# Optimization experiments

Measured on AMD Instinct MI355X. Metric: run time of the kernel, lower is better.

## Reference

```python
import jax, jax.numpy as jnp
import numpy as np

NUM_HEADS = 8
H_DIM = 24
COORDS_DIM = 3
NUM_W_PER_DIST = 8
BLOCK_SIZE = 128
N_HASHES = 3
N = 32768
HASH_DIM = H_DIM + (COORDS_DIM - 1) + 2  # q/k augmented with RPE coordinate terms


def layernorm(x, g, b, eps=1e-5):
    mu = x.mean(-1, keepdims=True)
    var = ((x - mu) ** 2).mean(-1, keepdims=True)
    return (x - mu) * jax.lax.rsqrt(var + eps) * g + b


def setup_inputs() -> dict:
    key = jax.random.key(0)
    ks = jax.random.split(key, 16)
    d, H = H_DIM, NUM_HEADS
    s = lambda i, shape, scale: jax.random.normal(ks[i], shape, jnp.float32) * scale
    return {
        "x": s(0, (N, d), 1.0),
        "coords": jax.random.uniform(ks[1], (N, COORDS_DIM), jnp.float32),
        "norm1_g": jnp.ones((d,), jnp.float32),
        "norm1_b": jnp.zeros((d,), jnp.float32),
        "Wq": s(2, (d, H * d), d ** -0.5),
        "Wk": s(3, (d, H * d), d ** -0.5),
        "Wv": s(4, (d, H * d), d ** -0.5),
        "w_rpe_W": s(5, (H * d, (COORDS_DIM - 1) * NUM_W_PER_DIST), 0.3),
        "Wo": s(6, (H * d, d), (H * d) ** -0.5),
        "bo": jnp.zeros((d,), jnp.float32),
        "norm2_g": jnp.ones((d,), jnp.float32),
        "norm2_b": jnp.zeros((d,), jnp.float32),
        "ff_W1": s(7, (d, d), d ** -0.5),
        "ff_b1": jnp.zeros((d,), jnp.float32),
        "ff_W2": s(8, (d, d), d ** -0.5),
        "ff_b2": jnp.zeros((d,), jnp.float32),
        "alphas": s(9, (N_HASHES, H, HASH_DIM), 1.0),  # E2LSH projection vectors
    }


def hept_attention(q, k, v, coords, w_rpe_W, alphas):
    # q,k,v: [n, H*d]. HEPT: fold RPE exp(-w*||dp||^2) into augmented q/k, then
    # n_hashes rounds of LSH sort + block-local attention, combined by softmax
    # over each round's log-normalizer (Reformer-style).
    n = q.shape[0]
    H, d, B = NUM_HEADS, H_DIM, BLOCK_SIZE
    nb = n // B
    q = q.reshape(n, H, d).transpose(1, 0, 2) * (d ** -0.5)  # [H,n,d]
    k = k.reshape(n, H, d).transpose(1, 0, 2)
    v = v.reshape(n, H, d).transpose(1, 0, 2)
    # per-head non-negative distance weights from w_rpe (mixture collapsed)
    Wm = w_rpe_W.reshape(H, d, COORDS_DIM - 1, NUM_W_PER_DIST)
    w = jnp.mean(Wm, axis=(1, 3)) ** 2                        # [H, c-1]
    p = coords[:, 1:]                                          # [n, c-1]
    sqn = jnp.einsum("hc,nc,nc->hn", w, p, p)                # w*||p||^2
    qp = jnp.sqrt(2.0) * jnp.sqrt(w)[:, None, :] * p[None]     # [H,n,c-1]
    ones = jnp.ones((H, n, 1), q.dtype)
    # q_hat.k_hat = q.k + 2*w*p_i.p_j - w|p_i|^2 - w|p_j|^2 = q.k - w*||p_i-p_j||^2
    q_hat = jnp.concatenate([q, qp, -sqn[..., None], ones], -1)  # [H,n,HASH_DIM]
    k_hat = jnp.concatenate([k, qp, ones, -sqn[..., None]], -1)
    outs, zs = [], []
    for r in range(N_HASHES):
        a = alphas[r]                                          # [H, HASH_DIM]
        iq = jnp.argsort(jnp.einsum("hne,he->hn", q_hat, a), -1)
        ik = jnp.argsort(jnp.einsum("hne,he->hn", k_hat, a), -1)
        qs = jnp.take_along_axis(q_hat, iq[..., None], 1).reshape(H, nb, B, -1)
        ks = jnp.take_along_axis(k_hat, ik[..., None], 1).reshape(H, nb, B, -1)
        vs = jnp.take_along_axis(v, ik[..., None], 1).reshape(H, nb, B, d)
        logits = jnp.einsum("hbqe,hbke->hbqk", qs, ks)         # [H,nb,B,B]
        z = jax.nn.logsumexp(logits, -1).reshape(H, n)
        o = jnp.einsum("hbqk,hbkd->hbqd", jax.nn.softmax(logits, -1), vs).reshape(H, n, d)
        inv = jnp.argsort(iq, -1)                              # unsort to input order
        outs.append(jnp.take_along_axis(o, inv[..., None], 1))
        zs.append(jnp.take_along_axis(z, inv, 1))
    wts = jax.nn.softmax(jnp.stack(zs), axis=0)[..., None]     # [R,H,n,1]
    out = (jnp.stack(outs) * wts).sum(0)                       # [H,n,d]
    return out.transpose(1, 0, 2).reshape(n, H * d)


def reference(x, coords, norm1_g, norm1_b, Wq, Wk, Wv, w_rpe_W, Wo, bo,
              norm2_g, norm2_b, ff_W1, ff_b1, ff_W2, ff_b2, alphas):
    xn = layernorm(x, norm1_g, norm1_b)
    q, k, v = xn @ Wq, xn @ Wk, xn @ Wv
    aggr = hept_attention(q, k, v, coords, w_rpe_W, alphas) @ Wo + bo
    x = x + aggr  # dropout is identity in eval mode
    h = layernorm(x, norm2_g, norm2_b)
    ff = jax.nn.relu(h @ ff_W1 + ff_b1) @ ff_W2 + ff_b2
    return x + ff
```

## Files before the change

kernel.cpp:

```cpp
#include <hip/hip_runtime.h>
#include <math.h>

#define NPT 32768
#define NH 8
#define HD 24
#define EDIM 28
#define NHASH 3
#define NSEG 48
#define NRH 24

typedef unsigned long long u64;
typedef unsigned short ushort;
typedef __attribute__((__vector_size__(8 * sizeof(short)))) short bf16x8;
typedef __attribute__((__vector_size__(4 * sizeof(float)))) float floatx4;
typedef __attribute__((__vector_size__(4 * sizeof(unsigned int)))) unsigned int uint32x4;

__device__ __forceinline__ ushort f2bf(float f) {
    unsigned u = __float_as_uint(f);
    unsigned r = u + 0x7FFF + ((u >> 16) & 1);
    return (ushort)(r >> 16);
}
__device__ __forceinline__ float us2f(ushort u) {
    return __uint_as_float(((unsigned)u) << 16);
}

__global__ __launch_bounds__(256) void k0b(
    const float* __restrict__ wrpe, const float* __restrict__ Wq,
    const float* __restrict__ Wk, const float* __restrict__ alphas,
    double* __restrict__ w64, double* __restrict__ cqp64,
    double* __restrict__ Aq, double* __restrict__ Ak, double* __restrict__ ct) {
    __shared__ double sw[16], sc[16];
    int t = threadIdx.x;
    if (t < 16) {
        int h = t >> 1, c = t & 1;
        double s = 0.0;
        for (int i = 0; i < 24; i++)
            for (int j = 0; j < 8; j++)
                s += (double)wrpe[(h * 24 + i) * 16 + c * 8 + j];
        double m = s / 192.0;
        sw[t] = m * m;
        sc[t] = sqrt(2.0) * fabs(m);
        w64[t] = sw[t];
        cqp64[t] = sc[t];
    }
    __syncthreads();
    const double QSCALE = 1.0 / sqrt(24.0);
    for (int idx = t; idx < 24 * NRH; idx += 256) {
        int i = idx / NRH, rh = idx % NRH;
        int h = rh & 7;
        double aq = 0.0, ak = 0.0;
        for (int e = 0; e < 24; e++) {
            double al = (double)alphas[rh * 28 + e];
            aq += (double)Wq[i * 192 + h * 24 + e] * al;
            ak += (double)Wk[i * 192 + h * 24 + e] * al;
        }
        Aq[idx] = aq * QSCALE;
        Ak[idx] = ak;
    }
    if (t < NRH) {
        int h = t & 7;
        ct[t * 4 + 0] = (double)alphas[t * 28 + 24] * sc[h * 2 + 0];
        ct[t * 4 + 1] = (double)alphas[t * 28 + 25] * sc[h * 2 + 1];
        ct[t * 4 + 2] = (double)alphas[t * 28 + 26];
        ct[t * 4 + 3] = (double)alphas[t * 28 + 27];
    }
}

__global__ __launch_bounds__(512) void k2s(
    const float* __restrict__ x, const float* __restrict__ n1g,
    const float* __restrict__ n1b, const float* __restrict__ coords,
    const double* __restrict__ Aq, const double* __restrict__ Ak,
    const double* __restrict__ ct, const double* __restrict__ w64,
    u64* __restrict__ keys, float* __restrict__ xnf) {
    __shared__ double sA[2][24][NRH];
    __shared__ double sCt[NRH][4];
    __shared__ double sW64[16];
    __shared__ double sGB[48];
    __shared__ double sXn[8][24];
    int t = threadIdx.x;
    for (int i = t; i < 24 * NRH; i += 512) sA[0][i / NRH][i % NRH] = Aq[i];
    for (int i = t; i < 24 * NRH; i += 512) sA[1][i / NRH][i % NRH] = Ak[i];
    for (int i = t; i < NRH * 4; i += 512) sCt[i / 4][i % 4] = ct[i];
    if (t < 16) sW64[t] = w64[t];
    if (t < 24) { sGB[t] = (double)n1g[t]; sGB[24 + t] = (double)n1b[t]; }
    __syncthreads();
    int wv = t >> 6, l = t & 63;
    for (int g = 0; g < 8; g++) {
        int n = blockIdx.x * 64 + g * 8 + wv;
        double xv = (l < 24) ? (double)x[(u64)n * 24 + l] : 0.0;
        double s = xv;
        s += __shfl_xor(s, 1); s += __shfl_xor(s, 2); s += __shfl_xor(s, 4);
        s += __shfl_xor(s, 8); s += __shfl_xor(s, 16);
        double mu = s / 24.0;
        double d = (l < 24) ? (xv - mu) : 0.0;
        double v2 = d * d;
        v2 += __shfl_xor(v2, 1); v2 += __shfl_xor(v2, 2); v2 += __shfl_xor(v2, 4);
        v2 += __shfl_xor(v2, 8); v2 += __shfl_xor(v2, 16);
        double rstd = 1.0 / sqrt(v2 / 24.0 + 1e-5);
        if (l < 24) {
            double xn = d * rstd * sGB[l] + sGB[24 + l];
            sXn[wv][l] = xn;
            xnf[(u64)n * 24 + l] = (float)xn;
        }
        double p0 = (double)coords[(u64)n * 3 + 1];
        double p1 = (double)coords[(u64)n * 3 + 2];
        if (l < 2 * NRH) {
            int qk = l / NRH, rh = l % NRH;
            int h = rh & 7;
            double sqn = sW64[2 * h] * p0 * p0 + sW64[2 * h + 1] * p1 * p1;
            double acc = sCt[rh][0] * p0 + sCt[rh][1] * p1;
            acc += qk ? (sCt[rh][2] - sqn * sCt[rh][3]) : (sCt[rh][3] - sqn * sCt[rh][2]);
            for (int i = 0; i < 24; i++) acc += sXn[wv][i] * sA[qk][i][rh];
            u64 u = (u64)__double_as_longlong(acc);
            if (u >> 63) u = ~u; else u |= 0x8000000000000000ULL;
            u64 key = (u & ~(u64)32767) | (u64)n;
            keys[(u64)l * NPT + n] = key;
        }
    }
}

__device__ __forceinline__ u64 shflx64(u64 v, int d) {
    int lo = __shfl_xor((int)(unsigned)v, d);
    int hi = __shfl_xor((int)(unsigned)(v >> 32), d);
    return ((u64)(unsigned)hi << 32) | (unsigned)lo;
}
__device__ __forceinline__ void cswap(u64& a, u64& b, bool up) {
    if ((a > b) == up) { u64 tmp = a; a = b; b = tmp; }
}
__device__ __forceinline__ u64* sslot(u64* s, int i) {
    int a = i << 3;
    a ^= ((a >> 9) & 7) << 4;
    return (u64*)((char*)s + a);
}
__device__ __forceinline__ void reg_passes(u64 e[8], int ib, int K, int jmax) {
    for (int j = jmax; j >= 1; j >>= 1) {
#pragma unroll
        for (int k = 0; k < 8; k++)
            if ((k & j) == 0) cswap(e[k], e[k | j], ((ib + k) & K) == 0);
    }
}
__device__ __forceinline__ void shfl_passes(u64 e[8], int t, int segoff, int K, int jhi, int jlo) {
    for (int j = jhi; j >= jlo; j >>= 1) {
        int d = j >> 3;
        bool lower = (t & d) == 0;
        bool up = ((segoff + ((t & ~d) << 3)) & K) == 0;
        bool keepmin = (lower == up);
#pragma unroll
        for (int k = 0; k < 8; k++) {
            u64 o = shflx64(e[k], d);
            bool ownsm = e[k] < o;
            e[k] = (ownsm == keepmin) ? e[k] : o;
        }
    }
}

#define K2P_PTS 32
#define INVLN2F 1.4426950408889634f
__global__ __launch_bounds__(1024) void k2p_sort(
    u64* keys,
    const float* __restrict__ xnf,
    const float* __restrict__ Wq, const float* __restrict__ Wk,
    const float* __restrict__ Wv, const float* __restrict__ coords,
    const double* __restrict__ w64, const double* __restrict__ cqp64,
    ushort* __restrict__ qhatB, ushort* __restrict__ khatB, ushort* __restrict__ varrB) {
    __shared__ __align__(16) char smem[65536];
    int t = threadIdx.x;
    if (blockIdx.x < 192) {
        u64* s = (u64*)smem;
        u64 gbase = (u64)blockIdx.x * 8192;
        int segoff = (int)(gbase & 32767);
        int ib = segoff + t * 8;
        u64 e[8];
#pragma unroll
        for (int k = 0; k < 8; k++) e[k] = keys[gbase + t * 8 + k];
        reg_passes(e, ib, 2, 1);
        reg_passes(e, ib, 4, 2);
        reg_passes(e, ib, 8, 4);
        for (int K = 16; K <= 512; K <<= 1) {
            shfl_passes(e, t, segoff, K, K >> 1, 8);
            reg_passes(e, ib, K, 4);
        }
#pragma unroll
        for (int k = 0; k < 8; k++) *sslot(s, t * 8 + k) = e[k];
        __syncthreads();
        for (int K = 1024; K <= 8192; K <<= 1) {
            for (int j = K >> 1; j >= 512; j >>= 1) {
                for (int p = t; p < 4096; p += 1024) {
                    int i = ((p & ~(j - 1)) << 1) | (p & (j - 1));
                    int i2 = i | j;
                    bool up = (((segoff + i) & K) == 0);
                    u64 a = *sslot(s, i), b = *sslot(s, i2);
                    if ((a > b) == up) { *sslot(s, i) = b; *sslot(s, i2) = a; }
                }
                __syncthreads();
            }
#pragma unroll
            for (int k = 0; k < 8; k++) e[k] = *sslot(s, t * 8 + k);
            shfl_passes(e, t, segoff, K, 256, 8);
            reg_passes(e, ib, K, 4);
            if (K < 8192) {
#pragma unroll
                for (int k = 0; k < 8; k++) *sslot(s, t * 8 + k) = e[k];
                __syncthreads();
            } else {
#pragma unroll
                for (int k = 0; k < 8; k++) keys[gbase + t * 8 + k] = e[k];
            }
        }
    } else {
        ushort* sT = (ushort*)smem;
        int n0 = (blockIdx.x - 192) * K2P_PTS;
        if (t < 576) {
            int m = t / 192, jj = t % 192;
            const float* W = (m == 0) ? Wq : ((m == 1) ? Wk : Wv);
            float wc[24];
#pragma unroll
            for (int i = 0; i < 24; i++) wc[i] = W[i * 192 + jj];
            const float scale = (m == 0) ? (float)(1.4426950408889634 / sqrt(24.0)) : 1.0f;
            int h = jj / 24, e = jj % 24;
            ushort* sbase = sT + ((m * 8 + h) * K2P_PTS) * 32 + e;
            for (int p = 0; p < K2P_PTS; p++) {
                int n = n0 + p;
                const float* xr = xnf + (u64)n * 24;
                float acc = 0.f;
#pragma unroll
                for (int i = 0; i < 24; i++) acc += xr[i] * wc[i];
                sbase[p * 32] = f2bf(acc * scale);
            }
        } else if (t < 640) {
            int l = t - 576;
            int h2 = l >> 3, e2 = 24 + (l & 7);
            double c0 = cqp64[h2 * 2], c1 = cqp64[h2 * 2 + 1];
            double wa = w64[h2 * 2], wb = w64[h2 * 2 + 1];
            ushort* qb = sT + ((0 * 8 + h2) * K2P_PTS) * 32 + e2;
            ushort* kb = sT + ((1 * 8 + h2) * K2P_PTS) * 32 + e2;
            ushort* vb = sT + ((2 * 8 + h2) * K2P_PTS) * 32 + e2;
            for (int p = 0; p < K2P_PTS; p++) {
                int n = n0 + p;
                double p0 = (double)coords[(u64)n * 3 + 1];
                double p1 = (double)coords[(u64)n * 3 + 2];
                float qv, kv;
                if (e2 < 26) {
                    int c = e2 - 24;
                    float qp = (float)((c ? c1 : c0) * (c ? p1 : p0));
                    qv = qp; kv = qp;
                } else if (e2 < 28) {
                    double sqn = wa * p0 * p0 + wb * p1 * p1;
                    if (e2 == 26) { qv = (float)(-sqn); kv = 1.0f; }
                    else          { qv = 1.0f; kv = (float)(-sqn); }
                } else {
                    qv = 0.0f; kv = 0.0f;
                }
                qb[p * 32] = f2bf(qv * INVLN2F);
                kb[p * 32] = f2bf(kv);
                vb[p * 32] = 0;
            }
        }
        __syncthreads();
        for (int c = t; c < 3 * 8 * K2P_PTS * 4; c += 1024) {
            int arrh = c >> 7, off = c & 127;
            int arr = arrh >> 3, hh = arrh & 7;
            uint32x4 v = *(const uint32x4*)(sT + arrh * (K2P_PTS * 32) + off * 8);
            ushort* op = (arr == 0) ? qhatB : ((arr == 1) ? khatB : varrB);
            *(uint32x4*)(op + (u64)hh * NPT * 32 + (u64)n0 * 32 + off * 8) = v;
        }
    }
}

__global__ __launch_bounds__(1024) void sort_tail1_fused(u64* keys) {
    __shared__ u64 s[8192];
    int t = threadIdx.x;
    u64 gbase = (u64)blockIdx.x * 8192;
    u64 pbase = gbase ^ 8192ULL;
    int ci = (int)((gbase >> 13) & 3);
    bool keepmin = (ci == 0) || (ci == 3);
    int segoff = (int)(gbase & 32767);
    int ib = segoff + t * 8;
    for (int i = t; i < 8192; i += 1024) {
        u64 a = keys[gbase + i];
        u64 b = keys[pbase + i];
        u64 mn = a < b ? a : b;
        u64 mx = a < b ? b : a;
        *sslot(s, i) = keepmin ? mn : mx;
    }
    __syncthreads();
    const int K = 16384;
    for (int j = 4096; j >= 512; j >>= 1) {
        for (int p = t; p < 4096; p += 1024) {
            int i = ((p & ~(j - 1)) << 1) | (p & (j - 1));
            int i2 = i | j;
            bool up = (((segoff + i) & K) == 0);
            u64 a = *sslot(s, i), b = *sslot(s, i2);
            if ((a > b) == up) { *sslot(s, i) = b; *sslot(s, i2) = a; }
        }
        __syncthreads();
    }
    u64 e[8];
#pragma unroll
    for (int k = 0; k < 8; k++) e[k] = *sslot(s, t * 8 + k);
    shfl_passes(e, t, segoff, K, 256, 8);
    reg_passes(e, ib, K, 4);
#pragma unroll
    for (int k = 0; k < 8; k++) keys[gbase + t * 8 + k] = e[k];
}

__global__ __launch_bounds__(1024) void sort_local_tail(u64* keys, int K, int minj) {
    __shared__ u64 s[8192];
    int t = threadIdx.x;
    u64 gbase = (u64)blockIdx.x * 8192;
    int segoff = (int)(gbase & 32767);
    int ib = segoff + t * 8;
    for (int i = t; i < 8192; i += 1024) *sslot(s, i) = keys[gbase + i];
    __syncthreads();
    for (int j = 4096; j >= 512; j >>= 1) {
        for (int p = t; p < 4096; p += 1024) {
            int i = ((p & ~(j - 1)) << 1) | (p & (j - 1));
            int i2 = i | j;
            bool up = (((segoff + i) & K) == 0);
            u64 a = *sslot(s, i), b = *sslot(s, i2);
            if ((a > b) == up) { *sslot(s, i) = b; *sslot(s, i2) = a; }
        }
        __syncthreads();
    }
    u64 e[8];
#pragma unroll
    for (int k = 0; k < 8; k++) e[k] = *sslot(s, t * 8 + k);
    shfl_passes(e, t, segoff, K, 256, minj >= 8 ? minj : 8);
    if (minj < 8) reg_passes(e, ib, K, 4);
#pragma unroll
    for (int k = 0; k < 8; k++) keys[gbase + t * 8 + k] = e[k];
}

__global__ void sort_global2(u64* keys) {
    int p = blockIdx.x * blockDim.x + threadIdx.x;
    if (p >= NSEG * 8192) return;
    int seg = p >> 13, c = p & 8191;
    u64 base = (u64)seg * 32768 + c;
    u64 e0 = keys[base];
    u64 e1 = keys[base + 8192];
    u64 e2 = keys[base + 16384];
    u64 e3 = keys[base + 24576];
    u64 tmp;
    if (e0 > e2) { tmp = e0; e0 = e2; e2 = tmp; }
    if (e1 > e3) { tmp = e1; e1 = e3; e3 = tmp; }
    if (e0 > e1) { tmp = e0; e0 = e1; e1 = tmp; }
    if (e2 > e3) { tmp = e2; e2 = e3; e3 = tmp; }
    keys[base] = e0;
    keys[base + 8192] = e1;
    keys[base + 16384] = e2;
    keys[base + 24576] = e3;
}

__global__ __launch_bounds__(256, 4) void k3_attn(
    const u64* __restrict__ keys, const ushort* __restrict__ qhatB,
    const ushort* __restrict__ khatB, const ushort* __restrict__ varrB,
    ushort* __restrict__ ozB) {
    int rh3 = blockIdx.x % 24;
    int b = blockIdx.x / 24;
    int h = rh3 & 7, r = rh3 >> 3;
    __shared__ __align__(16) char smem[6144 + 32768 + 512];
    char* sVt = smem;
    char* sP  = smem + 6144;
    ushort* qidx = (ushort*)(smem + 6144 + 32768);
    ushort* kidx = qidx + 128;
    int t = threadIdx.x;
    int segQ = r * 8 + h, segK = 24 + r * 8 + h;
    if (t < 128) {
        qidx[t] = (ushort)(keys[(u64)segQ * NPT + b * 128 + t] & 32767ULL);
    } else {
        int i = t - 128;
        kidx[i] = (ushort)(keys[(u64)segK * NPT + b * 128 + i] & 32767ULL);
    }
    __syncthreads();

    int wave = t >> 6, L = t & 63;
    int quad = L >> 4, n16 = L & 15;

    const bf16x8* Qg = (const bf16x8*)(qhatB + (u64)h * NPT * 32);
    const bf16x8* Kg = (const bf16x8*)(khatB + (u64)h * NPT * 32);
    bf16x8 afr[2];
#pragma unroll
    for (int rtg = 0; rtg < 2; rtg++) {
        int qi = qidx[wave * 32 + rtg * 16 + n16];
        afr[rtg] = Qg[(u64)qi * 4 + quad];
    }
    bf16x8 bfr[8];
#pragma unroll
    for (int ct = 0; ct < 8; ct++) {
        int ki = kidx[ct * 16 + n16];
        bfr[ct] = Kg[(u64)ki * 4 + quad];
    }
    if (t < 128) {
        int ki = kidx[t];
        const bf16x8* vr = (const bf16x8*)(varrB + ((u64)h * NPT + ki) * 32);
        bf16x8 v0 = vr[0], v1 = vr[1], v2 = vr[2];
        int colb = ((t & 15) << 4) | ((t >> 4) << 1);
#pragma unroll
        for (int e = 0; e < 8; e++) {
            int e0 = e, e1 = 8 + e, e2 = 16 + e;
            *(short*)(sVt + e0 * 256 + (colb ^ ((e0 & 7) << 4))) = v0[e];
            *(short*)(sVt + e1 * 256 + (colb ^ ((e1 & 7) << 4))) = v1[e];
            *(short*)(sVt + e2 * 256 + (colb ^ ((e2 & 7) << 4))) = v2[e];
        }
    }
    __syncthreads();

    floatx4 acc[2][8];
#pragma unroll
    for (int rtg = 0; rtg < 2; rtg++)
#pragma unroll
        for (int ct = 0; ct < 8; ct++)
            acc[rtg][ct] = (floatx4){0.f, 0.f, 0.f, 0.f};
#pragma unroll
    for (int ct = 0; ct < 8; ct++) {
#pragma unroll
        for (int rtg = 0; rtg < 2; rtg++)
            acc[rtg][ct] = __builtin_amdgcn_mfma_f32_16x16x32_bf16(afr[rtg], bfr[ct], acc[rtg][ct], 0, 0, 0);
    }

    float mrow[2][4], srow[2][4];
#pragma unroll
    for (int rtg = 0; rtg < 2; rtg++) {
#pragma unroll
        for (int rg = 0; rg < 4; rg++) {
            float m = acc[rtg][0][rg];
#pragma unroll
            for (int ct = 1; ct < 8; ct++) m = fmaxf(m, acc[rtg][ct][rg]);
            m = fmaxf(m, __shfl_xor(m, 1));
            m = fmaxf(m, __shfl_xor(m, 2));
            m = fmaxf(m, __shfl_xor(m, 4));
            m = fmaxf(m, __shfl_xor(m, 8));
            mrow[rtg][rg] = m;
            float p[8];
            float s = 0.0f;
#pragma unroll
            for (int ct = 0; ct < 8; ct++) {
                p[ct] = exp2f(acc[rtg][ct][rg] - m);
                s += p[ct];
            }
            s += __shfl_xor(s, 1);
            s += __shfl_xor(s, 2);
            s += __shfl_xor(s, 4);
            s += __shfl_xor(s, 8);
            srow[rtg][rg] = s;
            unsigned w0, w1, w2, w3;
            asm("v_cvt_pk_bf16_f32 %0, %1, %2" : "=v"(w0) : "v"(p[0]), "v"(p[1]));
            asm("v_cvt_pk_bf16_f32 %0, %1, %2" : "=v"(w1) : "v"(p[2]), "v"(p[3]));
            asm("v_cvt_pk_bf16_f32 %0, %1, %2" : "=v"(w2) : "v"(p[4]), "v"(p[5]));
            asm("v_cvt_pk_bf16_f32 %0, %1, %2" : "=v"(w3) : "v"(p[6]), "v"(p[7]));
            int row = wave * 32 + rtg * 16 + quad * 4 + rg;
            uint32x4 pk = {w0, w1, w2, w3};
            *(uint32x4*)(sP + row * 256 + (((n16 << 4)) ^ ((row & 7) << 4))) = pk;
        }
    }

    floatx4 occ[2][2];
#pragma unroll
    for (int rtg = 0; rtg < 2; rtg++)
#pragma unroll
        for (int ct2 = 0; ct2 < 2; ct2++)
            occ[rtg][ct2] = (floatx4){0.f, 0.f, 0.f, 0.f};
#pragma unroll
    for (int ks = 0; ks < 4; ks++) {
        int kb = ks * 64 + quad * 16;
        bf16x8 bv[2], av[2];
#pragma unroll
        for (int ct2 = 0; ct2 < 2; ct2++) {
            int e = ct2 * 16 + n16;
            int ec = (e < 24) ? e : 0;
            bv[ct2] = *(const bf16x8*)(sVt + ec * 256 + (kb ^ ((ec & 7) << 4)));
        }
#pragma unroll
        for (int rtg = 0; rtg < 2; rtg++) {
            int rowA = wave * 32 + rtg * 16 + n16;
            av[rtg] = *(const bf16x8*)(sP + rowA * 256 + (kb ^ ((rowA & 7) << 4)));
        }
#pragma unroll
        for (int rtg = 0; rtg < 2; rtg++)
#pragma unroll
            for (int ct2 = 0; ct2 < 2; ct2++)
                occ[rtg][ct2] = __builtin_amdgcn_mfma_f32_16x16x32_bf16(av[rtg], bv[ct2], occ[rtg][ct2], 0, 0, 0);
    }

    const float LN2F = 0.6931471805599453f;
#pragma unroll
    for (int rtg = 0; rtg < 2; rtg++) {
#pragma unroll
        for (int rg = 0; rg < 4; rg++) {
            int row = wave * 32 + rtg * 16 + quad * 4 + rg;
            int oi = qidx[row];
            float inv = 1.0f / srow[rtg][rg];
            ushort* orow = ozB + ((u64)segQ * NPT + oi) * 32;
#pragma unroll
            for (int ct2 = 0; ct2 < 2; ct2++) {
                int col = ct2 * 16 + n16;
                if (col < 24) orow[col] = f2bf(occ[rtg][ct2][rg] * inv);
            }
            if (n16 == 0)
                *(float*)(orow + 24) = mrow[rtg][rg] * LN2F + __logf(srow[rtg][rg]);
        }
    }
}

#define K4PTS 32
#define AT_STR 196
#define W_STR 28
__global__ __launch_bounds__(256) void k4_final(
    const ushort* __restrict__ ozB,
    const float* __restrict__ x,
    const float* __restrict__ Wo, const float* __restrict__ bo,
    const float* __restrict__ g2, const float* __restrict__ b2,
    const float* __restrict__ W1, const float* __restrict__ b1f,
    const float* __restrict__ W2, const float* __restrict__ b2f,
    float* __restrict__ out) {
    __shared__ __align__(16) float sWoT[24][AT_STR];
    __shared__ __align__(16) float sW1T[24][W_STR], sW2T[24][W_STR];
    __shared__ float sB[5 * 24];
    __shared__ __align__(16) float attn[K4PTS][AT_STR];
    __shared__ float xrow[K4PTS][25];
    __shared__ __align__(16) float h2row[K4PTS][W_STR];
    __shared__ __align__(16) float ffrow[K4PTS][W_STR];
    int t = threadIdx.x;
    int base = blockIdx.x * K4PTS;
    for (int i = t; i < 4608; i += 256) sWoT[i % 24][i / 24] = Wo[i];
    for (int i = t; i < 576; i += 256) {
        sW1T[i % 24][i / 24] = W1[i];
        sW2T[i % 24][i / 24] = W2[i];
    }
    if (t < 24) {
        sB[t] = bo[t]; sB[24 + t] = g2[t]; sB[48 + t] = b2[t];
        sB[72 + t] = b1f[t]; sB[96 + t] = b2f[t];
    }
    if (t < K4PTS * 4) {
        int p = t >> 2, c = 24 + (t & 3);
        h2row[p][c] = 0.f; ffrow[p][c] = 0.f;
    }
    if (t < 24 * 4) {
        int rr = t >> 2, c = 24 + (t & 3);
        sW1T[rr][c] = 0.f; sW2T[rr][c] = 0.f;
    }
    {
        int p = t >> 3, h = t & 7;
        int n = base + p;
        const ushort* r0 = ozB + ((u64)(0 * 8 + h) * NPT + n) * 32;
        const ushort* r1 = ozB + ((u64)(1 * 8 + h) * NPT + n) * 32;
        const ushort* r2 = ozB + ((u64)(2 * 8 + h) * NPT + n) * 32;
        float z0 = *(const float*)(r0 + 24);
        float z1 = *(const float*)(r1 + 24);
        float z2 = *(const float*)(r2 + 24);
        float zm = fmaxf(z0, fmaxf(z1, z2));
        float e0 = __expf(z0 - zm), e1 = __expf(z1 - zm), e2 = __expf(z2 - zm);
        float inv = 1.0f / (e0 + e1 + e2);
        float w0 = e0 * inv, w1 = e1 * inv, w2 = e2 * inv;
#pragma unroll
        for (int e = 0; e < 24; e++)
            attn[p][h * 24 + e] = w0 * us2f(r0[e]) + w1 * us2f(r1[e]) + w2 * us2f(r2[e]);
    }
    __syncthreads();
    int p = t >> 3, oe = t & 7;
    int n = base + p;
    {
        const floatx4* ap = (const floatx4*)&attn[p][0];
        const floatx4* w0p = (const floatx4*)&sWoT[oe][0];
        const floatx4* w1p = (const floatx4*)&sWoT[oe + 8][0];
        const floatx4* w2p = (const floatx4*)&sWoT[oe + 16][0];
        floatx4 A0 = {0.f, 0.f, 0.f, 0.f}, A1 = A0, A2 = A0;
        for (int ii = 0; ii < 48; ii++) {
            floatx4 av = ap[ii];
            A0 += av * w0p[ii];
            A1 += av * w1p[ii];
            A2 += av * w2p[ii];
        }
        float a0 = A0[0] + A0[1] + A0[2] + A0[3];
        float a1 = A1[0] + A1[1] + A1[2] + A1[3];
        float a2 = A2[0] + A2[1] + A2[2] + A2[3];
        xrow[p][oe]      = x[n * 24 + oe]      + a0 + sB[oe];
        xrow[p][oe + 8]  = x[n * 24 + oe + 8]  + a1 + sB[oe + 8];
        xrow[p][oe + 16] = x[n * 24 + oe + 16] + a2 + sB[oe + 16];
    }
    float mu, rstd;
    {
        float s = xrow[p][oe] + xrow[p][oe + 8] + xrow[p][oe + 16];
        s += __shfl_xor(s, 1); s += __shfl_xor(s, 2); s += __shfl_xor(s, 4);
        mu = s / 24.0f;
        float v0 = xrow[p][oe] - mu, v1 = xrow[p][oe + 8] - mu, v2 = xrow[p][oe + 16] - mu;
        float v = v0 * v0 + v1 * v1 + v2 * v2;
        v += __shfl_xor(v, 1); v += __shfl_xor(v, 2); v += __shfl_xor(v, 4);
        rstd = 1.0f / sqrtf(v / 24.0f + 1e-5f);
    }
    h2row[p][oe]      = (xrow[p][oe] - mu)      * rstd * sB[24 + oe]      + sB[48 + oe];
    h2row[p][oe + 8]  = (xrow[p][oe + 8] - mu)  * rstd * sB[24 + oe + 8]  + sB[48 + oe + 8];
    h2row[p][oe + 16] = (xrow[p][oe + 16] - mu) * rstd * sB[24 + oe + 16] + sB[48 + oe + 16];
    {
        const floatx4* hp = (const floatx4*)&h2row[p][0];
        const floatx4* w0p = (const floatx4*)&sW1T[oe][0];
        const floatx4* w1p = (const floatx4*)&sW1T[oe + 8][0];
        const floatx4* w2p = (const floatx4*)&sW1T[oe + 16][0];
        floatx4 A0 = {0.f, 0.f, 0.f, 0.f}, A1 = A0, A2 = A0;
#pragma unroll
        for (int ii = 0; ii < 6; ii++) {
            floatx4 hv = hp[ii];
            A0 += hv * w0p[ii];
            A1 += hv * w1p[ii];
            A2 += hv * w2p[ii];
        }
        ffrow[p][oe]      = fmaxf(A0[0]+A0[1]+A0[2]+A0[3] + sB[72 + oe], 0.f);
        ffrow[p][oe + 8]  = fmaxf(A1[0]+A1[1]+A1[2]+A1[3] + sB[72 + oe + 8], 0.f);
        ffrow[p][oe + 16] = fmaxf(A2[0]+A2[1]+A2[2]+A2[3] + sB[72 + oe + 16], 0.f);
    }
    {
        const floatx4* fp = (const floatx4*)&ffrow[p][0];
        const floatx4* w0p = (const floatx4*)&sW2T[oe][0];
        const floatx4* w1p = (const floatx4*)&sW2T[oe + 8][0];
        const floatx4* w2p = (const floatx4*)&sW2T[oe + 16][0];
        floatx4 A0 = {0.f, 0.f, 0.f, 0.f}, A1 = A0, A2 = A0;
#pragma unroll
        for (int ii = 0; ii < 6; ii++) {
            floatx4 fv = fp[ii];
            A0 += fv * w0p[ii];
            A1 += fv * w1p[ii];
            A2 += fv * w2p[ii];
        }
        out[n * 24 + oe]      = xrow[p][oe]      + A0[0]+A0[1]+A0[2]+A0[3] + sB[96 + oe];
        out[n * 24 + oe + 8]  = xrow[p][oe + 8]  + A1[0]+A1[1]+A1[2]+A1[3] + sB[96 + oe + 8];
        out[n * 24 + oe + 16] = xrow[p][oe + 16] + A2[0]+A2[1]+A2[2]+A2[3] + sB[96 + oe + 16];
    }
}

extern "C" void kernel_launch(void* const* d_in, const int* in_sizes, int n_in,
                              void* d_out, int out_size, void* d_ws, size_t ws_size,
                              hipStream_t stream) {
    const float* x      = (const float*)d_in[0];
    const float* coords = (const float*)d_in[1];
    const float* n1g    = (const float*)d_in[2];
    const float* n1b    = (const float*)d_in[3];
    const float* Wq     = (const float*)d_in[4];
    const float* Wk     = (const float*)d_in[5];
    const float* Wv     = (const float*)d_in[6];
    const float* wrpe   = (const float*)d_in[7];
    const float* Wo     = (const float*)d_in[8];
    const float* bo     = (const float*)d_in[9];
    const float* n2g    = (const float*)d_in[10];
    const float* n2b    = (const float*)d_in[11];
    const float* W1     = (const float*)d_in[12];
    const float* b1     = (const float*)d_in[13];
    const float* W2     = (const float*)d_in[14];
    const float* b2     = (const float*)d_in[15];
    const float* alphas = (const float*)d_in[16];

    char* ws = (char*)d_ws;
    size_t off = 0;
    auto alloc = [&](size_t bytes) -> void* {
        void* p = ws + off;
        off = (off + bytes + 255) & ~(size_t)255;
        return p;
    };
    double* w64   = (double*)alloc(256);
    double* cqp   = (double*)alloc(256);
    double* Aq    = (double*)alloc(24 * NRH * 8);
    double* Ak    = (double*)alloc(24 * NRH * 8);
    double* ct    = (double*)alloc(NRH * 4 * 8);
    float*  xnf   = (float*)alloc((size_t)NPT * 24 * 4);
    ushort* qhatB = (ushort*)alloc((size_t)NH * NPT * 32 * 2);
    ushort* khatB = (ushort*)alloc((size_t)NH * NPT * 32 * 2);
    ushort* varrB = (ushort*)alloc((size_t)NH * NPT * 32 * 2);
    u64*    keys  = (u64*)alloc((size_t)NSEG * NPT * 8);
    ushort* ozB   = (ushort*)alloc((size_t)NHASH * NH * NPT * 32 * 2);
    if (off > ws_size) return;

    k0b<<<1, 256, 0, stream>>>(wrpe, Wq, Wk, alphas, w64, cqp, Aq, Ak, ct);
    k2s<<<NPT / 64, 512, 0, stream>>>(x, n1g, n1b, coords, Aq, Ak, ct, w64, keys, xnf);
    k2p_sort<<<192 + NPT / K2P_PTS, 1024, 0, stream>>>(keys, xnf, Wq, Wk, Wv, coords,
                                                       w64, cqp, qhatB, khatB, varrB);
    sort_tail1_fused<<<192, 1024, 0, stream>>>(keys);
    sort_global2<<<NSEG * 8192 / 256, 256, 0, stream>>>(keys);
    sort_local_tail<<<192, 1024, 0, stream>>>(keys, 32768, 128);
    k3_attn<<<256 * 8 * 3, 256, 0, stream>>>(keys, qhatB, khatB, varrB, ozB);
    k4_final<<<NPT / K4PTS, 256, 0, stream>>>(ozB, x, Wo, bo, n2g, n2b,
                                              W1, b1, W2, b2, (float*)d_out);
}
```

Baseline: 289.7 us.

## Replace final bitonic merge stages with co-rank based parallel merge

The last bitonic merge of each 32768-key segment (a global compare-exchange pass plus a shared-memory local tail pass) is replaced by a merge-path kernel. Each 128-thread block binary-searches the co-rank of its output range across the two sorted halves (the second half read reversed, since bitonic leaves it descending) and writes its 128 merged keys into a new buffer. This turns two launches with many synchronised passes into one launch with a single read and write per key. The cost is an extra 12 MB workspace buffer and uncoalesced binary-search reads, and correctness depends on the halves being sorted in opposite directions.

```diff
diff --git a/kernel.cpp b/kernel.cpp
--- a/kernel.cpp
+++ b/kernel.cpp
@@ -304,51 +304,37 @@
     for (int k = 0; k < 8; k++) keys[gbase + t * 8 + k] = e[k];
 }
 
-__global__ __launch_bounds__(1024) void sort_local_tail(u64* keys, int K, int minj) {
-    __shared__ u64 s[8192];
+__device__ __forceinline__ int corank(int r, const u64* __restrict__ A,
+                                      const u64* __restrict__ B) {
+    int lo = r - 16384; if (lo < 0) lo = 0;
+    int hi = r < 16384 ? r : 16384;
+    while (lo < hi) {
+        int a = (lo + hi + 1) >> 1;
+        int b = r - a;
+        u64 Bv = B[16383 - b];
+        if (A[a - 1] < Bv) lo = a; else hi = a - 1;
+    }
+    return lo;
+}
+__global__ __launch_bounds__(128) void sort_corank(const u64* __restrict__ keys,
+                                                   u64* __restrict__ keys2) {
+    __shared__ int sh[2];
+    int seg = blockIdx.x >> 8;
+    int g = blockIdx.x & 255;
+    const u64* A = keys + (u64)seg * 32768;
+    const u64* B = A + 16384;
     int t = threadIdx.x;
-    u64 gbase = (u64)blockIdx.x * 8192;
-    int segoff = (int)(gbase & 32767);
-    int ib = segoff + t * 8;
-    for (int i = t; i < 8192; i += 1024) *sslot(s, i) = keys[gbase + i];
+    int r0 = g * 128;
+    if (t == 0)  sh[0] = corank(r0, A, B);
+    if (t == 64) sh[1] = corank(r0 + 128, A, B);
     __syncthreads();
-    for (int j = 4096; j >= 512; j >>= 1) {
-        for (int p = t; p < 4096; p += 1024) {
-            int i = ((p & ~(j - 1)) << 1) | (p & (j - 1));
-            int i2 = i | j;
-            bool up = (((segoff + i) & K) == 0);
-            u64 a = *sslot(s, i), b = *sslot(s, i2);
-            if ((a > b) == up) { *sslot(s, i) = b; *sslot(s, i2) = a; }
-        }
-        __syncthreads();
-    }
-    u64 e[8];
-#pragma unroll
-    for (int k = 0; k < 8; k++) e[k] = *sslot(s, t * 8 + k);
-    shfl_passes(e, t, segoff, K, 256, minj >= 8 ? minj : 8);
-    if (minj < 8) reg_passes(e, ib, K, 4);
-#pragma unroll
-    for (int k = 0; k < 8; k++) keys[gbase + t * 8 + k] = e[k];
-}
-
-__global__ void sort_global2(u64* keys) {
-    int p = blockIdx.x * blockDim.x + threadIdx.x;
-    if (p >= NSEG * 8192) return;
-    int seg = p >> 13, c = p & 8191;
-    u64 base = (u64)seg * 32768 + c;
-    u64 e0 = keys[base];
-    u64 e1 = keys[base + 8192];
-    u64 e2 = keys[base + 16384];
-    u64 e3 = keys[base + 24576];
-    u64 tmp;
-    if (e0 > e2) { tmp = e0; e0 = e2; e2 = tmp; }
-    if (e1 > e3) { tmp = e1; e1 = e3; e3 = tmp; }
-    if (e0 > e1) { tmp = e0; e0 = e1; e1 = tmp; }
-    if (e2 > e3) { tmp = e2; e2 = e3; e3 = tmp; }
-    keys[base] = e0;
-    keys[base + 8192] = e1;
-    keys[base + 16384] = e2;
-    keys[base + 24576] = e3;
+    int aLo = sh[0], aHi = sh[1];
+    int na = aHi - aLo;
+    int bLo = r0 - aLo;
+    u64 v;
+    if (t < na) v = A[aLo + t];
+    else        v = B[16383 - (bLo + (t - na))];
+    keys2[(u64)seg * 32768 + r0 + t] = v;
 }
 
 __global__ __launch_bounds__(256, 4) void k3_attn(
@@ -665,6 +651,7 @@
     ushort* khatB = (ushort*)alloc((size_t)NH * NPT * 32 * 2);
     ushort* varrB = (ushort*)alloc((size_t)NH * NPT * 32 * 2);
     u64*    keys  = (u64*)alloc((size_t)NSEG * NPT * 8);
+    u64*    keys2 = (u64*)alloc((size_t)NSEG * NPT * 8);
     ushort* ozB   = (ushort*)alloc((size_t)NHASH * NH * NPT * 32 * 2);
     if (off > ws_size) return;
 
@@ -673,9 +660,8 @@
     k2p_sort<<<192 + NPT / K2P_PTS, 1024, 0, stream>>>(keys, xnf, Wq, Wk, Wv, coords,
                                                        w64, cqp, qhatB, khatB, varrB);
     sort_tail1_fused<<<192, 1024, 0, stream>>>(keys);
-    sort_global2<<<NSEG * 8192 / 256, 256, 0, stream>>>(keys);
-    sort_local_tail<<<192, 1024, 0, stream>>>(keys, 32768, 128);
-    k3_attn<<<256 * 8 * 3, 256, 0, stream>>>(keys, qhatB, khatB, varrB, ozB);
+    sort_corank<<<NSEG * 256, 128, 0, stream>>>(keys, keys2);
+    k3_attn<<<256 * 8 * 3, 256, 0, stream>>>(keys2, qhatB, khatB, varrB, ozB);
     k4_final<<<NPT / K4PTS, 256, 0, stream>>>(ozB, x, Wo, bo, n2g, n2b,
                                               W1, b1, W2, b2, (float*)d_out);
 }
```

Measured after the change: 292.3 us. About the same (+0.9%).
